# Kernel tuning notes

Measured on AMD Instinct MI355X. Metric: run time of the kernel, lower is better.

The kernel has to match this reference:

```python
import jax, jax.numpy as jnp
import numpy as np

N, T, D_FEAT, D_GATE, D_MODEL = 1024, 32, 158, 63, 256
T_NHEAD, S_NHEAD, BETA = 4, 2, 5.0


def _pe(seq_len, d_model):
    pos = np.arange(seq_len, dtype=np.float32)[:, None]
    div = np.exp(np.arange(0, d_model, 2, dtype=np.float32) * (-np.log(10000.0) / d_model))
    pe = np.zeros((seq_len, d_model), np.float32)
    pe[:, 0::2] = np.sin(pos * div)
    pe[:, 1::2] = np.cos(pos * div)
    return jnp.asarray(pe)


def _ln(x, g, b):
    m = jnp.mean(x, -1, keepdims=True)
    v = jnp.var(x, -1, keepdims=True)
    return (x - m) / jnp.sqrt(v + 1e-5) * g + b


def _attn_block(x, n1g, n1b, Wq, Wk, Wv, n2g, n2b, W1, b1, W2, b2, nhead, over_stocks):
    # Faithful to SAttention/TAttention: per-head split of equally-sized dims is
    # equivalent to a single batched multi-head attention. Dropout p=0 (eval).
    n, t, d = x.shape
    dh = d // nhead
    temp = float(np.sqrt(d / nhead))
    xn = _ln(x, n1g, n1b)
    q = (xn @ Wq).reshape(n, t, nhead, dh)
    k = (xn @ Wk).reshape(n, t, nhead, dh)
    v = (xn @ Wv).reshape(n, t, nhead, dh)
    if over_stocks:
        # attention across stocks, per time step: scores [T,H,N,N]
        s = jnp.einsum('qthd,kthd->thqk', q, k) / temp
        a = jax.nn.softmax(s, -1)
        o = jnp.einsum('thqk,kthd->qthd', a, v).reshape(n, t, d)
    else:
        # attention across time, per stock: scores [N,H,T,T]
        s = jnp.einsum('nqhd,nkhd->nhqk', q, k) / temp
        a = jax.nn.softmax(s, -1)
        o = jnp.einsum('nhqk,nkhd->nqhd', a, v).reshape(n, t, d)
    xt = _ln(xn + o, n2g, n2b)
    ffn = jnp.maximum(xt @ W1 + b1, 0.0) @ W2 + b2
    return xt + ffn


def _forward(x, gate_W, gate_b, feat_W, feat_b, ds_mid_W, ds_mid_b, ds_small_W, ds_small_b,
             tn1g, tn1b, tWq, tWk, tWv, tn2g, tn2b, tW1, tb1, tW2, tb2,
             sn1g, sn1b, sWq, sWk, sWv, sn2g, sn2b, sW1, sb1, sW2, sb2,
             temp_W, fus_W, fus_b, fus_g, fus_bb, dec_W, dec_b):
    src = x[:, :, :D_FEAT]                       # [N,T,158]
    gate_in = x[:, -1, D_FEAT:]                  # [N,63] market features at last step
    g = D_FEAT * jax.nn.softmax((gate_in @ gate_W + gate_b) / BETA, -1)
    src = src * g[:, None, :]
    h = src @ feat_W + feat_b + _pe(T, D_MODEL)  # [N,32,256]
    # multi-scale downsampling: AvgPool1d k=2/s=2 and k=4/s=4 along time
    h_mid = h.reshape(N, T // 2, 2, D_MODEL).mean(2) @ ds_mid_W + ds_mid_b
    h_small = h.reshape(N, T // 4, 4, D_MODEL).mean(2) @ ds_small_W + ds_small_b
    pooled = []
    for hs in (h, h_mid, h_small):
        z = _attn_block(hs, tn1g, tn1b, tWq, tWk, tWv, tn2g, tn2b, tW1, tb1, tW2, tb2,
                        T_NHEAD, over_stocks=False)
        z = _attn_block(z, sn1g, sn1b, sWq, sWk, sWv, sn2g, sn2b, sW1, sb1, sW2, sb2,
                        S_NHEAD, over_stocks=True)
        # TemporalAttention pooling: query = last-step projection
        hh = z @ temp_W
        lam = jax.nn.softmax(jnp.einsum('ntd,nd->nt', hh, hh[:, -1, :]), -1)
        pooled.append(jnp.einsum('nt,ntd->nd', lam, z))
    fused = jnp.concatenate(pooled, -1) @ fus_W + fus_b
    fused = jnp.maximum(_ln(fused, fus_g, fus_bb), 0.0)
    return (fused @ dec_W + dec_b).squeeze(-1)    # [N]


def setup_inputs() -> dict:
    key = jax.random.key(0)
    ks = iter(jax.random.split(key, 40))
    w = lambda shape: jax.random.normal(next(ks), shape, jnp.float32) * 0.02
    d = D_MODEL
    inp = {
        'x': jax.random.normal(next(ks), (N, T, D_FEAT + D_GATE), jnp.float32),
        'gate_W': w((D_GATE, D_FEAT)), 'gate_b': jnp.zeros((D_FEAT,), jnp.float32),
        'feat_W': w((D_FEAT, d)), 'feat_b': jnp.zeros((d,), jnp.float32),
        'ds_mid_W': w((d, d)), 'ds_mid_b': jnp.zeros((d,), jnp.float32),
        'ds_small_W': w((d, d)), 'ds_small_b': jnp.zeros((d,), jnp.float32),
        'tn1g': jnp.ones((d,), jnp.float32), 'tn1b': jnp.zeros((d,), jnp.float32),
        'tWq': w((d, d)), 'tWk': w((d, d)), 'tWv': w((d, d)),
        'tn2g': jnp.ones((d,), jnp.float32), 'tn2b': jnp.zeros((d,), jnp.float32),
        'tW1': w((d, d)), 'tb1': jnp.zeros((d,), jnp.float32),
        'tW2': w((d, d)), 'tb2': jnp.zeros((d,), jnp.float32),
        'sn1g': jnp.ones((d,), jnp.float32), 'sn1b': jnp.zeros((d,), jnp.float32),
        'sWq': w((d, d)), 'sWk': w((d, d)), 'sWv': w((d, d)),
        'sn2g': jnp.ones((d,), jnp.float32), 'sn2b': jnp.zeros((d,), jnp.float32),
        'sW1': w((d, d)), 'sb1': jnp.zeros((d,), jnp.float32),
        'sW2': w((d, d)), 'sb2': jnp.zeros((d,), jnp.float32),
        'temp_W': w((d, d)),
        'fus_W': w((3 * d, d)), 'fus_b': jnp.zeros((d,), jnp.float32),
        'fus_g': jnp.ones((d,), jnp.float32), 'fus_bb': jnp.zeros((d,), jnp.float32),
        'dec_W': w((d, 1)), 'dec_b': jnp.zeros((1,), jnp.float32),
    }
    return inp


def reference(x, gate_W, gate_b, feat_W, feat_b, ds_mid_W, ds_mid_b, ds_small_W, ds_small_b,
              tn1g, tn1b, tWq, tWk, tWv, tn2g, tn2b, tW1, tb1, tW2, tb2,
              sn1g, sn1b, sWq, sWk, sWv, sn2g, sn2b, sW1, sb1, sW2, sb2,
              temp_W, fus_W, fus_b, fus_g, fus_bb, dec_W, dec_b):
    return _forward(x, gate_W, gate_b, feat_W, feat_b, ds_mid_W, ds_mid_b, ds_small_W, ds_small_b,
                    tn1g, tn1b, tWq, tWk, tWv, tn2g, tn2b, tW1, tb1, tW2, tb2,
                    sn1g, sn1b, sWq, sWk, sWv, sn2g, sn2b, sW1, sb1, sW2, sb2,
                    temp_W, fus_W, fus_b, fus_g, fus_bb, dec_W, dec_b)
```

## Files before the change

### kernel.cpp

```cpp
#include <hip/hip_runtime.h>
#include <math.h>

#define NS 1024
#define T0 32
#define DF 158
#define DG 63
#define DM 256
#define XROW (DF + DG)
#define MTOT 57344
#define B1R 32768
#define B2R 49152

typedef unsigned short u16;
typedef __attribute__((ext_vector_type(8))) short bf16x8_t;
typedef __attribute__((ext_vector_type(4))) float f32x4_t;

union frag_u {
  bf16x8_t f;
  unsigned short us[8];
  unsigned int u32[4];
};

__device__ inline unsigned short f2bf(float x) {
  unsigned int u = __float_as_uint(x);
  unsigned int r = u + 0x7fffu + ((u >> 16) & 1u);
  return (unsigned short)(r >> 16);
}
__device__ inline unsigned int pkbf(float lo, float hi) {
  return (unsigned int)f2bf(lo) | ((unsigned int)f2bf(hi) << 16);
}
__device__ inline float bf2f(u16 u) {
  return __uint_as_float(((unsigned int)u) << 16);
}
__device__ inline unsigned int cvtpk(float a, float b) {
  unsigned int r;
  asm("v_cvt_pk_bf16_f32 %0, %1, %2" : "=v"(r) : "v"(a), "v"(b));
  return r;
}

__global__ void k_pe(float* __restrict__ pe) {
  int t = blockIdx.x, d = threadIdx.x;
  int i2 = d & ~1;
  float div = expf((float)i2 * (-logf(10000.0f) / (float)DM));
  float ang = (float)t * div;
  pe[t * DM + d] = (d & 1) ? cosf(ang) : sinf(ang);
}

__global__ void k_gate(const float* __restrict__ x, const float* __restrict__ gW,
                       const float* __restrict__ gb, float* __restrict__ g) {
  int n = blockIdx.x, tid = threadIdx.x;
  __shared__ float gin[DG];
  __shared__ float red[256];
  if (tid < DG) gin[tid] = x[(size_t)n * T0 * XROW + 31 * XROW + DF + tid];
  __syncthreads();
  float myv = 0.f;
  if (tid < DF) {
    float acc = gb[tid];
    for (int j = 0; j < DG; j++) acc = fmaf(gin[j], gW[j * DF + tid], acc);
    myv = acc * (1.0f / 5.0f);
  }
  red[tid] = (tid < DF) ? myv : -1e30f;
  __syncthreads();
  for (int s = 128; s > 0; s >>= 1) { if (tid < s) red[tid] = fmaxf(red[tid], red[tid + s]); __syncthreads(); }
  float mx = red[0];
  __syncthreads();
  float e = (tid < DF) ? expf(myv - mx) : 0.f;
  red[tid] = e;
  __syncthreads();
  for (int s = 128; s > 0; s >>= 1) { if (tid < s) red[tid] += red[tid + s]; __syncthreads(); }
  float sum = red[0];
  if (tid < DF) g[(size_t)n * DF + tid] = (float)DF * e / sum;
}

struct WPrep { const float* s[14]; };
__global__ __launch_bounds__(256) void k_wprep(WPrep w, u16* __restrict__ dst) {
  int mat = blockIdx.x >> 4, nb = blockIdx.x & 15;
  int tid = threadIdx.x;
  int n = nb * 16 + (tid >> 4);
  int kc = (tid & 15) * 16;
  const float* src = w.s[mat];
  int K = (mat == 0) ? DF : 256;
  frag_u f0, f1;
#pragma unroll
  for (int j = 0; j < 8; j++) {
    int k0 = kc + j, k1 = kc + 8 + j;
    f0.us[j] = (k0 < K) ? f2bf(src[(size_t)k0 * 256 + n]) : (u16)0;
    f1.us[j] = (k1 < K) ? f2bf(src[(size_t)k1 * 256 + n]) : (u16)0;
  }
  u16* d = dst + (size_t)mat * 65536 + (size_t)n * 256 + kc;
  *(bf16x8_t*)d = f0.f;
  *(bf16x8_t*)(d + 8) = f1.f;
}

__global__ __launch_bounds__(256) void k_wtrans(const float* __restrict__ W, u16* __restrict__ Wt) {
  __shared__ u16 Ts[64][65];
  int k0 = blockIdx.x * 64, n0 = blockIdx.y * 64;
  int tid = threadIdx.x;
#pragma unroll
  for (int i = 0; i < 16; i++) {
    int e = tid + i * 256;
    int r = e >> 6, c = e & 63;
    Ts[r][c] = f2bf(W[(size_t)(k0 + r) * 256 + n0 + c]);
  }
  __syncthreads();
#pragma unroll
  for (int i = 0; i < 16; i++) {
    int e = tid + i * 256;
    int r = e >> 6, c = e & 63;
    Wt[(size_t)(n0 + r) * 768 + k0 + c] = Ts[c][r];
  }
}

template <bool BIAS, bool RELU, bool RES, bool OUTBF>
__global__ __launch_bounds__(256) void k_bgemm(
    const u16* __restrict__ A,
    const u16* __restrict__ B0, const u16* __restrict__ B1, const u16* __restrict__ B2,
    const float* __restrict__ bias, const u16* __restrict__ res,
    void* __restrict__ C0, void* __restrict__ C1, void* __restrict__ C2) {
  __shared__ __align__(16) unsigned char sm[32768];
  unsigned char* As = sm;
  unsigned char* Bs = sm + 16384;
  const u16* Bt = blockIdx.z == 0 ? B0 : (blockIdx.z == 1 ? B1 : B2);
  void* Cv = blockIdx.z == 0 ? C0 : (blockIdx.z == 1 ? C1 : C2);
  int m0 = blockIdx.y * 128, n0w = blockIdx.x * 128;
  int tid = threadIdx.x, lane = tid & 63, wid = tid >> 6;
  int qi = lane & 15, g = lane >> 4;
  int wr = wid >> 1, wc = wid & 1;
  f32x4_t acc[4][4];
#pragma unroll
  for (int i = 0; i < 4; i++)
#pragma unroll
    for (int j = 0; j < 4; j++) acc[i][j] = (f32x4_t){0.f, 0.f, 0.f, 0.f};
  for (int kt = 0; kt < 4; kt++) {
    if (kt) __syncthreads();
#pragma unroll
    for (int i = 0; i < 4; i++) {
      int cid = tid + i * 256;
      int row = cid >> 3, c = cid & 7;
      int swz = (c * 16) ^ ((row & 7) << 4);
      bf16x8_t va = *(const bf16x8_t*)(A + (size_t)(m0 + row) * 256 + kt * 64 + c * 8);
      *(bf16x8_t*)(As + row * 128 + swz) = va;
      bf16x8_t vb = *(const bf16x8_t*)(Bt + (size_t)(n0w + row) * 256 + kt * 64 + c * 8);
      *(bf16x8_t*)(Bs + row * 128 + swz) = vb;
    }
    __syncthreads();
    bf16x8_t Af[2][4], Bf[2][4];
#pragma unroll
    for (int mi = 0; mi < 4; mi++) {
      int row = wr * 64 + mi * 16 + qi;
      int swz = (row & 7) << 4;
      const unsigned char* ap = As + row * 128;
      Af[0][mi] = *(const bf16x8_t*)(ap + ((g * 16) ^ swz));
      Af[1][mi] = *(const bf16x8_t*)(ap + ((64 + g * 16) ^ swz));
    }
#pragma unroll
    for (int ni = 0; ni < 4; ni++) {
      int row = wc * 64 + ni * 16 + qi;
      int swz = (row & 7) << 4;
      const unsigned char* bp = Bs + row * 128;
      Bf[0][ni] = *(const bf16x8_t*)(bp + ((g * 16) ^ swz));
      Bf[1][ni] = *(const bf16x8_t*)(bp + ((64 + g * 16) ^ swz));
    }
#pragma unroll
    for (int ks = 0; ks < 2; ks++)
#pragma unroll
      for (int mi = 0; mi < 4; mi++)
#pragma unroll
        for (int ni = 0; ni < 4; ni++)
          acc[mi][ni] = __builtin_amdgcn_mfma_f32_16x16x32_bf16(Af[ks][mi], Bf[ks][ni], acc[mi][ni], 0, 0, 0);
  }
#pragma unroll
  for (int mi = 0; mi < 4; mi++) {
#pragma unroll
    for (int ni = 0; ni < 4; ni++) {
#pragma unroll
      for (int r = 0; r < 4; r++) {
        int row = m0 + wr * 64 + mi * 16 + 4 * g + r;
        int col = n0w + wc * 64 + ni * 16 + qi;
        float vv = acc[mi][ni][r];
        if (BIAS) vv += bias[col];
        if (RES) vv += bf2f(res[(size_t)row * 256 + col]);
        if (RELU) vv = fmaxf(vv, 0.f);
        if (OUTBF) ((u16*)Cv)[(size_t)row * 256 + col] = f2bf(vv);
        else ((float*)Cv)[(size_t)row * 256 + col] = vv;
      }
    }
  }
}

__global__ __launch_bounds__(256) void k_fgemm(
    const float* __restrict__ x, const float* __restrict__ gate,
    const u16* __restrict__ Bt, const float* __restrict__ bias,
    const float* __restrict__ pe, float* __restrict__ C) {
  __shared__ __align__(16) unsigned char sm[32768];
  unsigned char* As = sm;
  unsigned char* Bs = sm + 16384;
  int m0 = blockIdx.y * 128, n0w = blockIdx.x * 128;
  int tid = threadIdx.x, lane = tid & 63, wid = tid >> 6;
  int qi = lane & 15, g = lane >> 4;
  int wr = wid >> 1, wc = wid & 1;
  f32x4_t acc[4][4];
#pragma unroll
  for (int i = 0; i < 4; i++)
#pragma unroll
    for (int j = 0; j < 4; j++) acc[i][j] = (f32x4_t){0.f, 0.f, 0.f, 0.f};
  for (int kt = 0; kt < 3; kt++) {
    if (kt) __syncthreads();
#pragma unroll
    for (int i = 0; i < 4; i++) {
      int cid = tid + i * 256;
      int row = cid >> 3, c = cid & 7;
      int swz = (c * 16) ^ ((row & 7) << 4);
      int gk0 = kt * 64 + c * 8;
      const float* xr = x + (size_t)(m0 + row) * XROW;
      const float* gr = gate + (size_t)((m0 + row) >> 5) * DF;
      frag_u f;
#pragma unroll
      for (int j = 0; j < 8; j++) {
        int gk = gk0 + j;
        f.us[j] = (gk < DF) ? f2bf(xr[gk] * gr[gk]) : (u16)0;
      }
      *(bf16x8_t*)(As + row * 128 + swz) = f.f;
      bf16x8_t vb = *(const bf16x8_t*)(Bt + (size_t)(n0w + row) * 256 + kt * 64 + c * 8);
      *(bf16x8_t*)(Bs + row * 128 + swz) = vb;
    }
    __syncthreads();
    bf16x8_t Af[2][4], Bf[2][4];
#pragma unroll
    for (int mi = 0; mi < 4; mi++) {
      int row = wr * 64 + mi * 16 + qi;
      int swz = (row & 7) << 4;
      const unsigned char* ap = As + row * 128;
      Af[0][mi] = *(const bf16x8_t*)(ap + ((g * 16) ^ swz));
      Af[1][mi] = *(const bf16x8_t*)(ap + ((64 + g * 16) ^ swz));
    }
#pragma unroll
    for (int ni = 0; ni < 4; ni++) {
      int row = wc * 64 + ni * 16 + qi;
      int swz = (row & 7) << 4;
      const unsigned char* bp = Bs + row * 128;
      Bf[0][ni] = *(const bf16x8_t*)(bp + ((g * 16) ^ swz));
      Bf[1][ni] = *(const bf16x8_t*)(bp + ((64 + g * 16) ^ swz));
    }
#pragma unroll
    for (int ks = 0; ks < 2; ks++)
#pragma unroll
      for (int mi = 0; mi < 4; mi++)
#pragma unroll
        for (int ni = 0; ni < 4; ni++)
          acc[mi][ni] = __builtin_amdgcn_mfma_f32_16x16x32_bf16(Af[ks][mi], Bf[ks][ni], acc[mi][ni], 0, 0, 0);
  }
#pragma unroll
  for (int mi = 0; mi < 4; mi++) {
#pragma unroll
    for (int ni = 0; ni < 4; ni++) {
#pragma unroll
      for (int r = 0; r < 4; r++) {
        int row = m0 + wr * 64 + mi * 16 + 4 * g + r;
        int col = n0w + wc * 64 + ni * 16 + qi;
        C[(size_t)row * 256 + col] = acc[mi][ni][r] + bias[col] + pe[(row & (T0 - 1)) * DM + col];
      }
    }
  }
}

__global__ __launch_bounds__(256) void k_fus(const u16* __restrict__ A, const u16* __restrict__ Bt,
                                             const float* __restrict__ bias, float* __restrict__ C) {
  __shared__ __align__(16) unsigned char sm[16384];
  unsigned char* As = sm;
  unsigned char* Bs = sm + 8192;
  int n0 = blockIdx.x * 64, m0 = blockIdx.y * 64;
  int tid = threadIdx.x, lane = tid & 63, wid = tid >> 6;
  int qi = lane & 15, g = lane >> 4;
  f32x4_t acc[4];
#pragma unroll
  for (int i = 0; i < 4; i++) acc[i] = (f32x4_t){0.f, 0.f, 0.f, 0.f};
  for (int kt = 0; kt < 12; kt++) {
    if (kt) __syncthreads();
#pragma unroll
    for (int i = 0; i < 2; i++) {
      int cid = tid + i * 256;
      int row = cid >> 3, c = cid & 7;
      int swz = (c * 16) ^ ((row & 7) << 4);
      *(bf16x8_t*)(As + row * 128 + swz) = *(const bf16x8_t*)(A + (size_t)(m0 + row) * 768 + kt * 64 + c * 8);
      *(bf16x8_t*)(Bs + row * 128 + swz) = *(const bf16x8_t*)(Bt + (size_t)(n0 + row) * 768 + kt * 64 + c * 8);
    }
    __syncthreads();
    int arow = wid * 16 + qi;
    int asw = (arow & 7) << 4;
    bf16x8_t Af0 = *(const bf16x8_t*)(As + arow * 128 + ((g * 16) ^ asw));
    bf16x8_t Af1 = *(const bf16x8_t*)(As + arow * 128 + ((64 + g * 16) ^ asw));
#pragma unroll
    for (int ni = 0; ni < 4; ni++) {
      int brow = ni * 16 + qi;
      int bsw = (brow & 7) << 4;
      bf16x8_t B0 = *(const bf16x8_t*)(Bs + brow * 128 + ((g * 16) ^ bsw));
      bf16x8_t B1 = *(const bf16x8_t*)(Bs + brow * 128 + ((64 + g * 16) ^ bsw));
      acc[ni] = __builtin_amdgcn_mfma_f32_16x16x32_bf16(Af0, B0, acc[ni], 0, 0, 0);
      acc[ni] = __builtin_amdgcn_mfma_f32_16x16x32_bf16(Af1, B1, acc[ni], 0, 0, 0);
    }
  }
#pragma unroll
  for (int ni = 0; ni < 4; ni++)
#pragma unroll
    for (int r = 0; r < 4; r++) {
      int row = m0 + wid * 16 + 4 * g + r;
      int col = n0 + ni * 16 + qi;
      C[(size_t)row * 256 + col] = acc[ni][r] + bias[col];
    }
}

template <bool RES, bool ABF>
__global__ __launch_bounds__(256) void k_ln(const void* __restrict__ a, const float* __restrict__ b,
                                            const float* __restrict__ g, const float* __restrict__ be,
                                            u16* __restrict__ out) {
  int row = blockIdx.x * 4 + (threadIdx.x >> 6);
  int lane = threadIdx.x & 63;
  size_t base = (size_t)row * DM + lane * 4;
  float v[4];
  if (ABF) {
    ushort4 u = *(const ushort4*)((const u16*)a + base);
    v[0] = bf2f(u.x); v[1] = bf2f(u.y); v[2] = bf2f(u.z); v[3] = bf2f(u.w);
  } else {
    f32x4_t t = *(const f32x4_t*)((const float*)a + base);
    v[0] = t[0]; v[1] = t[1]; v[2] = t[2]; v[3] = t[3];
  }
  if (RES) {
    f32x4_t t = *(const f32x4_t*)(b + base);
    v[0] += t[0]; v[1] += t[1]; v[2] += t[2]; v[3] += t[3];
  }
  float s = v[0] + v[1] + v[2] + v[3];
#pragma unroll
  for (int off = 1; off < 64; off <<= 1) s += __shfl_xor(s, off);
  float mean = s * (1.0f / DM);
  float d0 = v[0] - mean, d1 = v[1] - mean, d2 = v[2] - mean, d3 = v[3] - mean;
  float ss = d0 * d0 + d1 * d1 + d2 * d2 + d3 * d3;
#pragma unroll
  for (int off = 1; off < 64; off <<= 1) ss += __shfl_xor(ss, off);
  float inv = rsqrtf(ss * (1.0f / DM) + 1e-5f);
  f32x4_t gg = *(const f32x4_t*)(g + lane * 4);
  f32x4_t bb = *(const f32x4_t*)(be + lane * 4);
  ushort4 o4;
  o4.x = f2bf(d0 * inv * gg[0] + bb[0]);
  o4.y = f2bf(d1 * inv * gg[1] + bb[1]);
  o4.z = f2bf(d2 * inv * gg[2] + bb[2]);
  o4.w = f2bf(d3 * inv * gg[3] + bb[3]);
  *(ushort4*)(out + base) = o4;
}

__global__ void k_poolmean(const float* __restrict__ h, u16* __restrict__ out, int Tout, int P) {
  int vi = blockIdx.x * 256 + threadIdx.x;
  int dv = vi & 63;
  int rowi = vi >> 6;
  int to = rowi % Tout;
  int n = rowi / Tout;
  int Tin = Tout * P;
  float s0 = 0.f, s1 = 0.f, s2 = 0.f, s3 = 0.f;
  for (int p = 0; p < P; p++) {
    f32x4_t t = *(const f32x4_t*)(h + ((size_t)(n * Tin + to * P + p)) * DM + dv * 4);
    s0 += t[0]; s1 += t[1]; s2 += t[2]; s3 += t[3];
  }
  float inv = 1.0f / (float)P;
  ushort4 o4;
  o4.x = f2bf(s0 * inv); o4.y = f2bf(s1 * inv); o4.z = f2bf(s2 * inv); o4.w = f2bf(s3 * inv);
  *(ushort4*)(out + (size_t)rowi * DM + dv * 4) = o4;
}

template <int T>
__global__ __launch_bounds__(256) void k_tattn(const u16* __restrict__ q, const u16* __restrict__ k,
                                               const u16* __restrict__ v, float* __restrict__ o) {
  constexpr int TR = (T < 16) ? 16 : T;
  constexpr int QKB = TR * 128;
  constexpr int HS = 2 * QKB + 64 * 80;
  __shared__ __align__(16) unsigned char smem[4 * HS];
  int n = blockIdx.x;
  int tid = threadIdx.x, lane = tid & 63, h = tid >> 6;
  int qi = lane & 15, g = lane >> 4;
  unsigned char* Qs = smem + h * HS;
  unsigned char* Ks = Qs + QKB;
  unsigned char* Vt = Ks + QKB;

  const u16* qh = q + (size_t)n * T * 256 + h * 64;
  const u16* kh = k + (size_t)n * T * 256 + h * 64;
  const u16* vh = v + (size_t)n * T * 256 + h * 64;
  const bf16x8_t zero8 = {0, 0, 0, 0, 0, 0, 0, 0};

  for (int idx = lane; idx < TR * 8; idx += 64) {
    int row = idx >> 3, c = idx & 7;
    bf16x8_t vq = zero8, vk = zero8;
    if (row < T) {
      vq = *(const bf16x8_t*)(qh + (size_t)row * 256 + c * 8);
      vk = *(const bf16x8_t*)(kh + (size_t)row * 256 + c * 8);
    }
    int off = row * 128 + ((c * 16) ^ ((row & 7) << 4));
    *(bf16x8_t*)(Qs + off) = vq;
    *(bf16x8_t*)(Ks + off) = vk;
  }
  {
    int kp = lane & 15, dg = lane >> 4;
    int d0 = dg * 16;
    int kk = 2 * kp;
    int cb = ((((kk >> 2) & 3) << 3) | (((kk >> 4) & 1) << 2) | (kk & 3)) * 2;
    frag_u a0, a1, b0, b1;
    a0.f = a1.f = b0.f = b1.f = zero8;
    if (kk < T) {
      a0.f = *(const bf16x8_t*)(vh + (size_t)kk * 256 + d0);
      a1.f = *(const bf16x8_t*)(vh + (size_t)kk * 256 + d0 + 8);
    }
    if (kk + 1 < T) {
      b0.f = *(const bf16x8_t*)(vh + (size_t)(kk + 1) * 256 + d0);
      b1.f = *(const bf16x8_t*)(vh + (size_t)(kk + 1) * 256 + d0 + 8);
    }
#pragma unroll
    for (int i = 0; i < 8; i++)
      *(unsigned int*)(Vt + (d0 + i) * 80 + cb) = (unsigned int)a0.us[i] | ((unsigned int)b0.us[i] << 16);
#pragma unroll
    for (int i = 0; i < 8; i++)
      *(unsigned int*)(Vt + (d0 + 8 + i) * 80 + cb) = (unsigned int)a1.us[i] | ((unsigned int)b1.us[i] << 16);
  }
  __syncthreads();

  constexpr int NQT = (T == 32) ? 2 : 1;
  constexpr int NSUB = (T == 32) ? 2 : 1;
  const float scale = 0.125f;

  bf16x8_t Qb[NQT][2];
#pragma unroll
  for (int qt = 0; qt < NQT; qt++) {
    int row = qt * 16 + qi;
    int sw = (row & 7) << 4;
#pragma unroll
    for (int kst = 0; kst < 2; kst++)
      Qb[qt][kst] = *(const bf16x8_t*)(Qs + row * 128 + ((kst * 64 + g * 16) ^ sw));
  }
  f32x4_t sacc[NQT][NSUB];
#pragma unroll
  for (int qt = 0; qt < NQT; qt++)
#pragma unroll
    for (int sub = 0; sub < NSUB; sub++) sacc[qt][sub] = (f32x4_t){0.f, 0.f, 0.f, 0.f};
#pragma unroll
  for (int sub = 0; sub < NSUB; sub++) {
    int row = sub * 16 + qi;
    int sw = (row & 7) << 4;
    bf16x8_t Ka[2];
#pragma unroll
    for (int kst = 0; kst < 2; kst++)
      Ka[kst] = *(const bf16x8_t*)(Ks + row * 128 + ((kst * 64 + g * 16) ^ sw));
#pragma unroll
    for (int qt = 0; qt < NQT; qt++)
#pragma unroll
      for (int kst = 0; kst < 2; kst++)
        sacc[qt][sub] = __builtin_amdgcn_mfma_f32_16x16x32_bf16(Ka[kst], Qb[qt][kst], sacc[qt][sub], 0, 0, 0);
  }
  frag_u Pf[NQT];
#pragma unroll
  for (int qt = 0; qt < NQT; qt++) {
    float sv[NSUB][4];
    float mx = -3.0e38f;
#pragma unroll
    for (int sub = 0; sub < NSUB; sub++)
#pragma unroll
      for (int r = 0; r < 4; r++) {
        int key = sub * 16 + 4 * g + r;
        float s = sacc[qt][sub][r] * scale;
        if (key >= T) s = -3.0e38f;
        sv[sub][r] = s;
        mx = fmaxf(mx, s);
      }
    mx = fmaxf(mx, __shfl_xor(mx, 16));
    mx = fmaxf(mx, __shfl_xor(mx, 32));
    float p[NSUB][4];
    float l = 0.f;
#pragma unroll
    for (int sub = 0; sub < NSUB; sub++)
#pragma unroll
      for (int r = 0; r < 4; r++) {
        float e = __expf(sv[sub][r] - mx);
        p[sub][r] = e;
        l += e;
      }
    l += __shfl_xor(l, 16);
    l += __shfl_xor(l, 32);
    float linv = 1.0f / l;
    Pf[qt].u32[0] = cvtpk(p[0][0] * linv, p[0][1] * linv);
    Pf[qt].u32[1] = cvtpk(p[0][2] * linv, p[0][3] * linv);
    if (NSUB == 2) {
      Pf[qt].u32[2] = cvtpk(p[NSUB - 1][0] * linv, p[NSUB - 1][1] * linv);
      Pf[qt].u32[3] = cvtpk(p[NSUB - 1][2] * linv, p[NSUB - 1][3] * linv);
    } else {
      Pf[qt].u32[2] = 0u;
      Pf[qt].u32[3] = 0u;
    }
  }
  f32x4_t oacc[NQT][4];
#pragma unroll
  for (int qt = 0; qt < NQT; qt++)
#pragma unroll
    for (int ni = 0; ni < 4; ni++) oacc[qt][ni] = (f32x4_t){0.f, 0.f, 0.f, 0.f};
#pragma unroll
  for (int ni = 0; ni < 4; ni++) {
    bf16x8_t Vb = *(const bf16x8_t*)(Vt + (ni * 16 + qi) * 80 + g * 16);
#pragma unroll
    for (int qt = 0; qt < NQT; qt++)
      oacc[qt][ni] = __builtin_amdgcn_mfma_f32_16x16x32_bf16(Pf[qt].f, Vb, oacc[qt][ni], 0, 0, 0);
  }
#pragma unroll
  for (int qt = 0; qt < NQT; qt++)
#pragma unroll
    for (int ni = 0; ni < 4; ni++)
#pragma unroll
      for (int r = 0; r < 4; r++) {
        int qq = qt * 16 + 4 * g + r;
        if (qq < T) o[((size_t)(n * T + qq)) * 256 + h * 64 + ni * 16 + qi] = oacc[qt][ni][r];
      }
}

__global__ __launch_bounds__(256) void k_sattn(const u16* __restrict__ q, const u16* __restrict__ k,
                                               const u16* __restrict__ v, float* __restrict__ o) {
  __shared__ __align__(16) unsigned char smem[32768];
  unsigned char* Ks = smem;
  unsigned char* Vt = smem + 16384;

  int bid = blockIdx.x;
  int T, rowbase;
  if (bid < 1024) { T = 32; rowbase = 0; }
  else if (bid < 1536) { T = 16; rowbase = B1R; bid -= 1024; }
  else { T = 8; rowbase = B2R; bid -= 1536; }
  const int NTH = T * 2;
  int xcd = bid & 7, slot = bid >> 3;
  int th = xcd * (NTH >> 3) + (slot >> 4);
  int qb = slot & 15;
  int t = th >> 1, h = th & 1;

  int tid = threadIdx.x;
  int lane = tid & 63;
  int wid = tid >> 6;
  int qi = lane & 15;
  int g = lane >> 4;
  const float invtemp = 0.08838834764831845f;

  const size_t rs = (size_t)T * 256;
  const size_t hb = (size_t)rowbase * 256 + (size_t)t * 256 + h * 128;
  const u16* qp = q + hb;
  const u16* kp = k + hb;
  const u16* vp = v + hb;
  float* op = o + hb;

  int q0 = qb * 64 + wid * 16;

  bf16x8_t Qf[4];
  {
    const u16* src = qp + (size_t)(q0 + qi) * rs + g * 8;
#pragma unroll
    for (int kst = 0; kst < 4; kst++) Qf[kst] = *(const bf16x8_t*)(src + kst * 32);
  }

  f32x4_t Oacc[8];
#pragma unroll
  for (int i = 0; i < 8; i++) Oacc[i] = (f32x4_t){0.f, 0.f, 0.f, 0.f};
  float mrun = -3.0e38f, lrun = 0.f;

  int kpair = tid & 31, dg = tid >> 5;
  int d0s = dg * 16;
  int kk = 2 * kpair;
  int cb = (((kk >> 5) << 5) | (((kk >> 2) & 3) << 3) | (((kk >> 4) & 1) << 2) | (kk & 3)) * 2;

  for (int kb = 0; kb < NS; kb += 64) {
    __syncthreads();
#pragma unroll
    for (int i = 0; i < 4; i++) {
      int cid = tid + i * 256;
      int row = cid >> 4, ch = cid & 15;
      bf16x8_t kv = *(const bf16x8_t*)(kp + (size_t)(kb + row) * rs + ch * 8);
      *(bf16x8_t*)(Ks + row * 256 + ((ch * 16) ^ ((row & 7) << 4))) = kv;
    }
    {
      const u16* s0 = vp + (size_t)(kb + kk) * rs + d0s;
      const u16* s1 = s0 + rs;
      frag_u a0, a1, b0, b1;
      a0.f = *(const bf16x8_t*)s0;
      a1.f = *(const bf16x8_t*)(s0 + 8);
      b0.f = *(const bf16x8_t*)s1;
      b1.f = *(const bf16x8_t*)(s1 + 8);
#pragma unroll
      for (int i = 0; i < 8; i++) {
        int d = d0s + i;
        *(unsigned int*)(Vt + d * 128 + (cb ^ ((d & 7) << 4))) =
            (unsigned int)a0.us[i] | ((unsigned int)b0.us[i] << 16);
      }
#pragma unroll
      for (int i = 0; i < 8; i++) {
        int d = d0s + 8 + i;
        *(unsigned int*)(Vt + d * 128 + (cb ^ ((d & 7) << 4))) =
            (unsigned int)a1.us[i] | ((unsigned int)b1.us[i] << 16);
      }
    }
    __syncthreads();

    f32x4_t sacc[4];
#pragma unroll
    for (int i = 0; i < 4; i++) sacc[i] = (f32x4_t){0.f, 0.f, 0.f, 0.f};
#pragma unroll
    for (int sub = 0; sub < 4; sub++) {
      int row = sub * 16 + qi;
      int swz = (row & 7) << 4;
      const unsigned char* kr = Ks + row * 256;
#pragma unroll
      for (int kst = 0; kst < 4; kst++) {
        bf16x8_t Af = *(const bf16x8_t*)(kr + ((g * 16 + kst * 64) ^ swz));
        sacc[sub] = __builtin_amdgcn_mfma_f32_16x16x32_bf16(Af, Qf[kst], sacc[sub], 0, 0, 0);
      }
    }

    float sv[4][4];
    float pmax = -3.0e38f;
#pragma unroll
    for (int sub = 0; sub < 4; sub++)
#pragma unroll
      for (int r = 0; r < 4; r++) {
        sv[sub][r] = sacc[sub][r] * invtemp;
        pmax = fmaxf(pmax, sv[sub][r]);
      }
    pmax = fmaxf(pmax, __shfl_xor(pmax, 16));
    pmax = fmaxf(pmax, __shfl_xor(pmax, 32));
    if (__any(pmax - mrun > 8.0f)) {
      float mnew = fmaxf(mrun, pmax);
      float fac = __expf(mrun - mnew);
      lrun *= fac;
      float fr[4];
#pragma unroll
      for (int r = 0; r < 4; r++) fr[r] = __shfl(fac, (g << 2) | r);
#pragma unroll
      for (int dsub = 0; dsub < 8; dsub++)
#pragma unroll
        for (int r = 0; r < 4; r++) Oacc[dsub][r] *= fr[r];
      mrun = mnew;
    }
    float p[4][4];
    float ls = 0.f;
#pragma unroll
    for (int sub = 0; sub < 4; sub++)
#pragma unroll
      for (int r = 0; r < 4; r++) {
        float e = __expf(sv[sub][r] - mrun);
        p[sub][r] = e;
        ls += e;
      }
    ls += __shfl_xor(ls, 16);
    ls += __shfl_xor(ls, 32);
    lrun += ls;

    frag_u pf0, pf1;
    pf0.u32[0] = cvtpk(p[0][0], p[0][1]);
    pf0.u32[1] = cvtpk(p[0][2], p[0][3]);
    pf0.u32[2] = cvtpk(p[1][0], p[1][1]);
    pf0.u32[3] = cvtpk(p[1][2], p[1][3]);
    pf1.u32[0] = cvtpk(p[2][0], p[2][1]);
    pf1.u32[1] = cvtpk(p[2][2], p[2][3]);
    pf1.u32[2] = cvtpk(p[3][0], p[3][1]);
    pf1.u32[3] = cvtpk(p[3][2], p[3][3]);

#pragma unroll
    for (int kst = 0; kst < 2; kst++) {
      bf16x8_t Pa = kst ? pf1.f : pf0.f;
#pragma unroll
      for (int dsub = 0; dsub < 8; dsub++) {
        int row = dsub * 16 + qi;
        bf16x8_t Vb = *(const bf16x8_t*)(Vt + row * 128 + ((g * 16 + kst * 64) ^ ((row & 7) << 4)));
        Oacc[dsub] = __builtin_amdgcn_mfma_f32_16x16x32_bf16(Pa, Vb, Oacc[dsub], 0, 0, 0);
      }
    }
  }

  float rin[4];
#pragma unroll
  for (int r = 0; r < 4; r++) rin[r] = 1.0f / __shfl(lrun, (g << 2) | r);
#pragma unroll
  for (int dsub = 0; dsub < 8; dsub++)
#pragma unroll
    for (int r = 0; r < 4; r++) {
      size_t row = (size_t)(q0 + 4 * g + r);
      op[row * rs + dsub * 16 + qi] = Oacc[dsub][r] * rin[r];
    }
}

__global__ __launch_bounds__(256) void k_tpool(const float* __restrict__ hh, const u16* __restrict__ z,
                                               u16* __restrict__ pooled, int T, int off) {
  int n = blockIdx.x, d = threadIdx.x;
  __shared__ float red[256];
  __shared__ float lam[T0];
  __shared__ float lame[T0];
  float last = hh[((size_t)(n * T + T - 1)) * DM + d];
  for (int t = 0; t < T; t++) {
    red[d] = hh[((size_t)(n * T + t)) * DM + d] * last;
    __syncthreads();
    for (int s = 128; s > 0; s >>= 1) { if (d < s) red[d] += red[d + s]; __syncthreads(); }
    if (d == 0) lam[t] = red[0];
    __syncthreads();
  }
  float mx = -1e30f;
  for (int t = 0; t < T; t++) mx = fmaxf(mx, lam[t]);
  if (d < T) lame[d] = expf(lam[d] - mx);
  __syncthreads();
  float sum = 0.f;
  for (int t = 0; t < T; t++) sum += lame[t];
  float acc = 0.f;
  for (int t = 0; t < T; t++) acc += lame[t] * bf2f(z[((size_t)(n * T + t)) * DM + d]);
  pooled[(size_t)n * 768 + off + d] = f2bf(acc / sum);
}

__global__ __launch_bounds__(256) void k_final(const float* __restrict__ f, const float* __restrict__ g,
                                               const float* __restrict__ b, const float* __restrict__ dw,
                                               const float* __restrict__ db, float* __restrict__ out) {
  int n = blockIdx.x, d = threadIdx.x;
  float v = f[(size_t)n * DM + d];
  __shared__ float red[256];
  red[d] = v;
  __syncthreads();
  for (int s = 128; s > 0; s >>= 1) { if (d < s) red[d] += red[d + s]; __syncthreads(); }
  float mean = red[0] * (1.0f / DM);
  __syncthreads();
  float dv = v - mean;
  red[d] = dv * dv;
  __syncthreads();
  for (int s = 128; s > 0; s >>= 1) { if (d < s) red[d] += red[d + s]; __syncthreads(); }
  float var = red[0] * (1.0f / DM);
  __syncthreads();
  float y = dv * rsqrtf(var + 1e-5f) * g[d] + b[d];
  y = fmaxf(y, 0.f);
  red[d] = y * dw[d];
  __syncthreads();
  for (int s = 128; s > 0; s >>= 1) { if (d < s) red[d] += red[d + s]; __syncthreads(); }
  if (d == 0) out[n] = red[0] + db[0];
}

extern "C" void kernel_launch(void* const* d_in, const int* in_sizes, int n_in,
                              void* d_out, int out_size, void* d_ws, size_t ws_size,
                              hipStream_t stream) {
  const float* x = (const float*)d_in[0];
  const float* gate_W = (const float*)d_in[1];
  const float* gate_b = (const float*)d_in[2];
  const float* feat_W = (const float*)d_in[3];
  const float* feat_b = (const float*)d_in[4];
  const float* ds_mid_W = (const float*)d_in[5];
  const float* ds_mid_b = (const float*)d_in[6];
  const float* ds_small_W = (const float*)d_in[7];
  const float* ds_small_b = (const float*)d_in[8];
  const float* tn1g = (const float*)d_in[9];
  const float* tn1b = (const float*)d_in[10];
  const float* tWq = (const float*)d_in[11];
  const float* tWk = (const float*)d_in[12];
  const float* tWv = (const float*)d_in[13];
  const float* tn2g = (const float*)d_in[14];
  const float* tn2b = (const float*)d_in[15];
  const float* tW1 = (const float*)d_in[16];
  const float* tb1 = (const float*)d_in[17];
  const float* tW2 = (const float*)d_in[18];
  const float* tb2 = (const float*)d_in[19];
  const float* sn1g = (const float*)d_in[20];
  const float* sn1b = (const float*)d_in[21];
  const float* sWq = (const float*)d_in[22];
  const float* sWk = (const float*)d_in[23];
  const float* sWv = (const float*)d_in[24];
  const float* sn2g = (const float*)d_in[25];
  const float* sn2b = (const float*)d_in[26];
  const float* sW1 = (const float*)d_in[27];
  const float* sb1 = (const float*)d_in[28];
  const float* sW2 = (const float*)d_in[29];
  const float* sb2 = (const float*)d_in[30];
  const float* temp_W = (const float*)d_in[31];
  const float* fus_W = (const float*)d_in[32];
  const float* fus_b = (const float*)d_in[33];
  const float* fus_g = (const float*)d_in[34];
  const float* fus_bb = (const float*)d_in[35];
  const float* dec_W = (const float*)d_in[36];
  const float* dec_b = (const float*)d_in[37];

  float* ws = (float*)d_ws;
  size_t o = 0;
  float* pe = ws + o; o += 8192;
  float* g = ws + o; o += 161792;
  u16* wt = (u16*)(ws + o); o += 458752;
  float* hcat = ws + o; o += (size_t)MTOT * 256;
  u16* bXNu = (u16*)(ws + o); o += (size_t)MTOT * 128;
  u16* bQu = (u16*)(ws + o); o += (size_t)MTOT * 128;
  u16* bKu = (u16*)(ws + o); o += (size_t)MTOT * 128;
  u16* bVu = (u16*)(ws + o); o += (size_t)MTOT * 128;
  float* bO = hcat;
  float* hh = hcat;
  float* fused = hcat;
  u16* pooledu = bXNu;
  u16* wFus = bKu;

  u16* wFeat = wt;
  u16* wDSm = wt + 1 * 65536;
  u16* wDSs = wt + 2 * 65536;
  u16* wTQ = wt + 3 * 65536;
  u16* wTK = wt + 4 * 65536;
  u16* wTV = wt + 5 * 65536;
  u16* wT1 = wt + 6 * 65536;
  u16* wT2 = wt + 7 * 65536;
  u16* wSQ = wt + 8 * 65536;
  u16* wSK = wt + 9 * 65536;
  u16* wSV = wt + 10 * 65536;
  u16* wS1 = wt + 11 * 65536;
  u16* wS2 = wt + 12 * 65536;
  u16* wTW = wt + 13 * 65536;

  k_pe<<<T0, DM, 0, stream>>>(pe);
  k_gate<<<NS, 256, 0, stream>>>(x, gate_W, gate_b, g);
  WPrep wp;
  wp.s[0] = feat_W; wp.s[1] = ds_mid_W; wp.s[2] = ds_small_W;
  wp.s[3] = tWq; wp.s[4] = tWk; wp.s[5] = tWv; wp.s[6] = tW1; wp.s[7] = tW2;
  wp.s[8] = sWq; wp.s[9] = sWk; wp.s[10] = sWv; wp.s[11] = sW1; wp.s[12] = sW2;
  wp.s[13] = temp_W;
  k_wprep<<<224, 256, 0, stream>>>(wp, wt);

  k_fgemm<<<dim3(2, 256), 256, 0, stream>>>(x, g, wFeat, feat_b, pe, hcat);
  k_poolmean<<<4096, 256, 0, stream>>>(hcat, bQu, 16, 2);
  k_bgemm<true, false, false, false><<<dim3(2, 128, 1), 256, 0, stream>>>(
      bQu, wDSm, wDSm, wDSm, ds_mid_b, nullptr, hcat + (size_t)B1R * 256, nullptr, nullptr);
  k_poolmean<<<2048, 256, 0, stream>>>(hcat, bQu, 8, 4);
  k_bgemm<true, false, false, false><<<dim3(2, 64, 1), 256, 0, stream>>>(
      bQu, wDSs, wDSs, wDSs, ds_small_b, nullptr, hcat + (size_t)B2R * 256, nullptr, nullptr);

  dim3 g1(2, MTOT / 128, 1), g3(2, MTOT / 128, 3);
  k_ln<false, false><<<MTOT / 4, 256, 0, stream>>>(hcat, nullptr, tn1g, tn1b, bXNu);
  k_bgemm<false, false, false, true><<<g3, 256, 0, stream>>>(
      bXNu, wTQ, wTK, wTV, nullptr, nullptr, bQu, bKu, bVu);
  k_tattn<32><<<NS, 256, 0, stream>>>(bQu, bKu, bVu, bO);
  k_tattn<16><<<NS, 256, 0, stream>>>(bQu + (size_t)B1R * 256, bKu + (size_t)B1R * 256,
                                      bVu + (size_t)B1R * 256, bO + (size_t)B1R * 256);
  k_tattn<8><<<NS, 256, 0, stream>>>(bQu + (size_t)B2R * 256, bKu + (size_t)B2R * 256,
                                     bVu + (size_t)B2R * 256, bO + (size_t)B2R * 256);
  k_ln<true, true><<<MTOT / 4, 256, 0, stream>>>(bXNu, bO, tn2g, tn2b, bQu);
  k_bgemm<true, true, false, true><<<g1, 256, 0, stream>>>(
      bQu, wT1, wT1, wT1, tb1, nullptr, bKu, nullptr, nullptr);
  k_bgemm<true, false, true, true><<<g1, 256, 0, stream>>>(
      bKu, wT2, wT2, wT2, tb2, bQu, bVu, nullptr, nullptr);
  k_ln<false, true><<<MTOT / 4, 256, 0, stream>>>(bVu, nullptr, sn1g, sn1b, bXNu);
  k_bgemm<false, false, false, true><<<g3, 256, 0, stream>>>(
      bXNu, wSQ, wSK, wSV, nullptr, nullptr, bQu, bKu, bVu);
  k_sattn<<<1792, 256, 0, stream>>>(bQu, bKu, bVu, bO);
  k_ln<true, true><<<MTOT / 4, 256, 0, stream>>>(bXNu, bO, sn2g, sn2b, bQu);
  k_bgemm<true, true, false, true><<<g1, 256, 0, stream>>>(
      bQu, wS1, wS1, wS1, sb1, nullptr, bKu, nullptr, nullptr);
  k_bgemm<true, false, true, true><<<g1, 256, 0, stream>>>(
      bKu, wS2, wS2, wS2, sb2, bQu, bVu, nullptr, nullptr);
  k_bgemm<false, false, false, false><<<g1, 256, 0, stream>>>(
      bVu, wTW, wTW, wTW, nullptr, nullptr, hh, nullptr, nullptr);
  k_tpool<<<NS, 256, 0, stream>>>(hh, bVu, pooledu, 32, 0);
  k_tpool<<<NS, 256, 0, stream>>>(hh + (size_t)B1R * 256, bVu + (size_t)B1R * 256, pooledu, 16, 256);
  k_tpool<<<NS, 256, 0, stream>>>(hh + (size_t)B2R * 256, bVu + (size_t)B2R * 256, pooledu, 8, 512);

  k_wtrans<<<dim3(12, 4), 256, 0, stream>>>(fus_W, wFus);
  k_fus<<<dim3(4, 16), 256, 0, stream>>>(pooledu, wFus, fus_b, fused);
  k_final<<<NS, 256, 0, stream>>>(fused, fus_g, fus_bb, dec_W, dec_b, (float*)d_out);
}
```

Before: 594.7 us.

## Fold softmax scale into Q weights, double sattn query tiles, async GEMM loads, warp-reduce tpool

Several independent changes land together. The attention temperature and log2(e) are folded into the bf16 Wq weights during prep, so both attention kernels can use exp2 without a per-score multiply. k_sattn now has each wave process two 16-row query tiles that share every K and V fragment read from LDS, which halves the grid and the K/V staging per query. The bgemm tile loads use global_load_lds with the XOR swizzle moved onto the source address. k_tpool replaces its serial block-wide reductions with wave shuffle reductions. Risks include higher register pressure in sattn, lower occupancy, and small rounding differences from pre-scaled bf16 weights.

```diff
diff --git a/kernel.cpp b/kernel.cpp
--- a/kernel.cpp
+++ b/kernel.cpp
@@ -26,9 +26,6 @@
   unsigned int r = u + 0x7fffu + ((u >> 16) & 1u);
   return (unsigned short)(r >> 16);
 }
-__device__ inline unsigned int pkbf(float lo, float hi) {
-  return (unsigned int)f2bf(lo) | ((unsigned int)f2bf(hi) << 16);
-}
 __device__ inline float bf2f(u16 u) {
   return __uint_as_float(((unsigned int)u) << 16);
 }
@@ -36,6 +33,10 @@
   unsigned int r;
   asm("v_cvt_pk_bf16_f32 %0, %1, %2" : "=v"(r) : "v"(a), "v"(b));
   return r;
+}
+__device__ inline void gl16(const u16* gp, unsigned char* lp) {
+  __builtin_amdgcn_global_load_lds((const __attribute__((address_space(1))) unsigned int*)gp,
+                                   (__attribute__((address_space(3))) unsigned int*)lp, 16, 0, 0);
 }
 
 __global__ void k_pe(float* __restrict__ pe) {
@@ -72,20 +73,21 @@
   if (tid < DF) g[(size_t)n * DF + tid] = (float)DF * e / sum;
 }
 
-struct WPrep { const float* s[14]; };
+struct WPrep { const float* s[14]; float sc[14]; };
 __global__ __launch_bounds__(256) void k_wprep(WPrep w, u16* __restrict__ dst) {
   int mat = blockIdx.x >> 4, nb = blockIdx.x & 15;
   int tid = threadIdx.x;
   int n = nb * 16 + (tid >> 4);
   int kc = (tid & 15) * 16;
   const float* src = w.s[mat];
+  float sc = w.sc[mat];
   int K = (mat == 0) ? DF : 256;
   frag_u f0, f1;
 #pragma unroll
   for (int j = 0; j < 8; j++) {
     int k0 = kc + j, k1 = kc + 8 + j;
-    f0.us[j] = (k0 < K) ? f2bf(src[(size_t)k0 * 256 + n]) : (u16)0;
-    f1.us[j] = (k1 < K) ? f2bf(src[(size_t)k1 * 256 + n]) : (u16)0;
+    f0.us[j] = (k0 < K) ? f2bf(src[(size_t)k0 * 256 + n] * sc) : (u16)0;
+    f1.us[j] = (k1 < K) ? f2bf(src[(size_t)k1 * 256 + n] * sc) : (u16)0;
   }
   u16* d = dst + (size_t)mat * 65536 + (size_t)n * 256 + kc;
   *(bf16x8_t*)d = f0.f;
@@ -137,11 +139,9 @@
     for (int i = 0; i < 4; i++) {
       int cid = tid + i * 256;
       int row = cid >> 3, c = cid & 7;
-      int swz = (c * 16) ^ ((row & 7) << 4);
-      bf16x8_t va = *(const bf16x8_t*)(A + (size_t)(m0 + row) * 256 + kt * 64 + c * 8);
-      *(bf16x8_t*)(As + row * 128 + swz) = va;
-      bf16x8_t vb = *(const bf16x8_t*)(Bt + (size_t)(n0w + row) * 256 + kt * 64 + c * 8);
-      *(bf16x8_t*)(Bs + row * 128 + swz) = vb;
+      int cs = c ^ (row & 7);
+      gl16(A + (size_t)(m0 + row) * 256 + kt * 64 + cs * 8, As + cid * 16);
+      gl16(Bt + (size_t)(n0w + row) * 256 + kt * 64 + cs * 8, Bs + cid * 16);
     }
     __syncthreads();
     bf16x8_t Af[2][4], Bf[2][4];
@@ -422,7 +422,6 @@
 
   constexpr int NQT = (T == 32) ? 2 : 1;
   constexpr int NSUB = (T == 32) ? 2 : 1;
-  const float scale = 0.125f;
 
   bf16x8_t Qb[NQT][2];
 #pragma unroll
@@ -462,7 +461,7 @@
 #pragma unroll
       for (int r = 0; r < 4; r++) {
         int key = sub * 16 + 4 * g + r;
-        float s = sacc[qt][sub][r] * scale;
+        float s = sacc[qt][sub][r];
         if (key >= T) s = -3.0e38f;
         sv[sub][r] = s;
         mx = fmaxf(mx, s);
@@ -475,7 +474,7 @@
     for (int sub = 0; sub < NSUB; sub++)
 #pragma unroll
       for (int r = 0; r < 4; r++) {
-        float e = __expf(sv[sub][r] - mx);
+        float e = exp2f(sv[sub][r] - mx);
         p[sub][r] = e;
         l += e;
       }
@@ -523,13 +522,13 @@
 
   int bid = blockIdx.x;
   int T, rowbase;
-  if (bid < 1024) { T = 32; rowbase = 0; }
-  else if (bid < 1536) { T = 16; rowbase = B1R; bid -= 1024; }
-  else { T = 8; rowbase = B2R; bid -= 1536; }
+  if (bid < 512) { T = 32; rowbase = 0; }
+  else if (bid < 768) { T = 16; rowbase = B1R; bid -= 512; }
+  else { T = 8; rowbase = B2R; bid -= 768; }
   const int NTH = T * 2;
   int xcd = bid & 7, slot = bid >> 3;
-  int th = xcd * (NTH >> 3) + (slot >> 4);
-  int qb = slot & 15;
+  int th = xcd * (NTH >> 3) + (slot >> 3);
+  int qb = slot & 7;
   int t = th >> 1, h = th & 1;
 
   int tid = threadIdx.x;
@@ -537,7 +536,6 @@
   int wid = tid >> 6;
   int qi = lane & 15;
   int g = lane >> 4;
-  const float invtemp = 0.08838834764831845f;
 
   const size_t rs = (size_t)T * 256;
   const size_t hb = (size_t)rowbase * 256 + (size_t)t * 256 + h * 128;
@@ -546,19 +544,26 @@
   const u16* vp = v + hb;
   float* op = o + hb;
 
-  int q0 = qb * 64 + wid * 16;
-
-  bf16x8_t Qf[4];
+  int q0 = qb * 128 + wid * 32;
+
+  bf16x8_t QfA[4], QfB[4];
   {
-    const u16* src = qp + (size_t)(q0 + qi) * rs + g * 8;
-#pragma unroll
-    for (int kst = 0; kst < 4; kst++) Qf[kst] = *(const bf16x8_t*)(src + kst * 32);
-  }
-
-  f32x4_t Oacc[8];
-#pragma unroll
-  for (int i = 0; i < 8; i++) Oacc[i] = (f32x4_t){0.f, 0.f, 0.f, 0.f};
-  float mrun = -3.0e38f, lrun = 0.f;
+    const u16* sA = qp + (size_t)(q0 + qi) * rs + g * 8;
+    const u16* sB = sA + 16 * rs;
+#pragma unroll
+    for (int kst = 0; kst < 4; kst++) {
+      QfA[kst] = *(const bf16x8_t*)(sA + kst * 32);
+      QfB[kst] = *(const bf16x8_t*)(sB + kst * 32);
+    }
+  }
+
+  f32x4_t OA[8], OB[8];
+#pragma unroll
+  for (int i = 0; i < 8; i++) {
+    OA[i] = (f32x4_t){0.f, 0.f, 0.f, 0.f};
+    OB[i] = (f32x4_t){0.f, 0.f, 0.f, 0.f};
+  }
+  float mA = -3.0e38f, lA = 0.f, mB = -3.0e38f, lB = 0.f;
 
   int kpair = tid & 31, dg = tid >> 5;
   int d0s = dg * 16;
@@ -597,9 +602,12 @@
     }
     __syncthreads();
 
-    f32x4_t sacc[4];
-#pragma unroll
-    for (int i = 0; i < 4; i++) sacc[i] = (f32x4_t){0.f, 0.f, 0.f, 0.f};
+    f32x4_t saA[4], saB[4];
+#pragma unroll
+    for (int i = 0; i < 4; i++) {
+      saA[i] = (f32x4_t){0.f, 0.f, 0.f, 0.f};
+      saB[i] = (f32x4_t){0.f, 0.f, 0.f, 0.f};
+    }
 #pragma unroll
     for (int sub = 0; sub < 4; sub++) {
       int row = sub * 16 + qi;
@@ -608,105 +616,146 @@
 #pragma unroll
       for (int kst = 0; kst < 4; kst++) {
         bf16x8_t Af = *(const bf16x8_t*)(kr + ((g * 16 + kst * 64) ^ swz));
-        sacc[sub] = __builtin_amdgcn_mfma_f32_16x16x32_bf16(Af, Qf[kst], sacc[sub], 0, 0, 0);
-      }
-    }
-
-    float sv[4][4];
-    float pmax = -3.0e38f;
+        saA[sub] = __builtin_amdgcn_mfma_f32_16x16x32_bf16(Af, QfA[kst], saA[sub], 0, 0, 0);
+        saB[sub] = __builtin_amdgcn_mfma_f32_16x16x32_bf16(Af, QfB[kst], saB[sub], 0, 0, 0);
+      }
+    }
+
+    float pmA = -3.0e38f, pmB = -3.0e38f;
 #pragma unroll
     for (int sub = 0; sub < 4; sub++)
 #pragma unroll
       for (int r = 0; r < 4; r++) {
-        sv[sub][r] = sacc[sub][r] * invtemp;
-        pmax = fmaxf(pmax, sv[sub][r]);
-      }
-    pmax = fmaxf(pmax, __shfl_xor(pmax, 16));
-    pmax = fmaxf(pmax, __shfl_xor(pmax, 32));
-    if (__any(pmax - mrun > 8.0f)) {
-      float mnew = fmaxf(mrun, pmax);
-      float fac = __expf(mrun - mnew);
-      lrun *= fac;
-      float fr[4];
-#pragma unroll
-      for (int r = 0; r < 4; r++) fr[r] = __shfl(fac, (g << 2) | r);
+        pmA = fmaxf(pmA, saA[sub][r]);
+        pmB = fmaxf(pmB, saB[sub][r]);
+      }
+    pmA = fmaxf(pmA, __shfl_xor(pmA, 16));
+    pmA = fmaxf(pmA, __shfl_xor(pmA, 32));
+    pmB = fmaxf(pmB, __shfl_xor(pmB, 16));
+    pmB = fmaxf(pmB, __shfl_xor(pmB, 32));
+    if (__any(fmaxf(pmA - mA, pmB - mB) > 11.5f)) {
+      float mnA = fmaxf(mA, pmA), mnB = fmaxf(mB, pmB);
+      float fA = exp2f(mA - mnA), fB = exp2f(mB - mnB);
+      lA *= fA;
+      lB *= fB;
+      float frA[4], frB[4];
+#pragma unroll
+      for (int r = 0; r < 4; r++) {
+        frA[r] = __shfl(fA, (g << 2) | r);
+        frB[r] = __shfl(fB, (g << 2) | r);
+      }
 #pragma unroll
       for (int dsub = 0; dsub < 8; dsub++)
 #pragma unroll
-        for (int r = 0; r < 4; r++) Oacc[dsub][r] *= fr[r];
-      mrun = mnew;
-    }
-    float p[4][4];
-    float ls = 0.f;
+        for (int r = 0; r < 4; r++) {
+          OA[dsub][r] *= frA[r];
+          OB[dsub][r] *= frB[r];
+        }
+      mA = mnA;
+      mB = mnB;
+    }
+    float pA[4][4], pB[4][4];
+    float lsA = 0.f, lsB = 0.f;
 #pragma unroll
     for (int sub = 0; sub < 4; sub++)
 #pragma unroll
       for (int r = 0; r < 4; r++) {
-        float e = __expf(sv[sub][r] - mrun);
-        p[sub][r] = e;
-        ls += e;
-      }
-    ls += __shfl_xor(ls, 16);
-    ls += __shfl_xor(ls, 32);
-    lrun += ls;
-
-    frag_u pf0, pf1;
-    pf0.u32[0] = cvtpk(p[0][0], p[0][1]);
-    pf0.u32[1] = cvtpk(p[0][2], p[0][3]);
-    pf0.u32[2] = cvtpk(p[1][0], p[1][1]);
-    pf0.u32[3] = cvtpk(p[1][2], p[1][3]);
-    pf1.u32[0] = cvtpk(p[2][0], p[2][1]);
-    pf1.u32[1] = cvtpk(p[2][2], p[2][3]);
-    pf1.u32[2] = cvtpk(p[3][0], p[3][1]);
-    pf1.u32[3] = cvtpk(p[3][2], p[3][3]);
+        float eA = exp2f(saA[sub][r] - mA);
+        float eB = exp2f(saB[sub][r] - mB);
+        pA[sub][r] = eA;
+        pB[sub][r] = eB;
+        lsA += eA;
+        lsB += eB;
+      }
+    lsA += __shfl_xor(lsA, 16);
+    lsA += __shfl_xor(lsA, 32);
+    lsB += __shfl_xor(lsB, 16);
+    lsB += __shfl_xor(lsB, 32);
+    lA += lsA;
+    lB += lsB;
+
+    frag_u fA0, fA1, fB0, fB1;
+    fA0.u32[0] = cvtpk(pA[0][0], pA[0][1]);
+    fA0.u32[1] = cvtpk(pA[0][2], pA[0][3]);
+    fA0.u32[2] = cvtpk(pA[1][0], pA[1][1]);
+    fA0.u32[3] = cvtpk(pA[1][2], pA[1][3]);
+    fA1.u32[0] = cvtpk(pA[2][0], pA[2][1]);
+    fA1.u32[1] = cvtpk(pA[2][2], pA[2][3]);
+    fA1.u32[2] = cvtpk(pA[3][0], pA[3][1]);
+    fA1.u32[3] = cvtpk(pA[3][2], pA[3][3]);
+    fB0.u32[0] = cvtpk(pB[0][0], pB[0][1]);
+    fB0.u32[1] = cvtpk(pB[0][2], pB[0][3]);
+    fB0.u32[2] = cvtpk(pB[1][0], pB[1][1]);
+    fB0.u32[3] = cvtpk(pB[1][2], pB[1][3]);
+    fB1.u32[0] = cvtpk(pB[2][0], pB[2][1]);
+    fB1.u32[1] = cvtpk(pB[2][2], pB[2][3]);
+    fB1.u32[2] = cvtpk(pB[3][0], pB[3][1]);
+    fB1.u32[3] = cvtpk(pB[3][2], pB[3][3]);
 
 #pragma unroll
     for (int kst = 0; kst < 2; kst++) {
-      bf16x8_t Pa = kst ? pf1.f : pf0.f;
+      bf16x8_t PaA = kst ? fA1.f : fA0.f;
+      bf16x8_t PaB = kst ? fB1.f : fB0.f;
 #pragma unroll
       for (int dsub = 0; dsub < 8; dsub++) {
         int row = dsub * 16 + qi;
         bf16x8_t Vb = *(const bf16x8_t*)(Vt + row * 128 + ((g * 16 + kst * 64) ^ ((row & 7) << 4)));
-        Oacc[dsub] = __builtin_amdgcn_mfma_f32_16x16x32_bf16(Pa, Vb, Oacc[dsub], 0, 0, 0);
-      }
-    }
-  }
-
-  float rin[4];
-#pragma unroll
-  for (int r = 0; r < 4; r++) rin[r] = 1.0f / __shfl(lrun, (g << 2) | r);
+        OA[dsub] = __builtin_amdgcn_mfma_f32_16x16x32_bf16(PaA, Vb, OA[dsub], 0, 0, 0);
+        OB[dsub] = __builtin_amdgcn_mfma_f32_16x16x32_bf16(PaB, Vb, OB[dsub], 0, 0, 0);
+      }
+    }
+  }
+
+  float rinA[4], rinB[4];
+#pragma unroll
+  for (int r = 0; r < 4; r++) {
+    rinA[r] = 1.0f / __shfl(lA, (g << 2) | r);
+    rinB[r] = 1.0f / __shfl(lB, (g << 2) | r);
+  }
 #pragma unroll
   for (int dsub = 0; dsub < 8; dsub++)
 #pragma unroll
     for (int r = 0; r < 4; r++) {
-      size_t row = (size_t)(q0 + 4 * g + r);
-      op[row * rs + dsub * 16 + qi] = Oacc[dsub][r] * rin[r];
+      size_t rowA = (size_t)(q0 + 4 * g + r);
+      op[rowA * rs + dsub * 16 + qi] = OA[dsub][r] * rinA[r];
+      op[(rowA + 16) * rs + dsub * 16 + qi] = OB[dsub][r] * rinB[r];
     }
 }
 
 __global__ __launch_bounds__(256) void k_tpool(const float* __restrict__ hh, const u16* __restrict__ z,
                                                u16* __restrict__ pooled, int T, int off) {
-  int n = blockIdx.x, d = threadIdx.x;
-  __shared__ float red[256];
+  int n = blockIdx.x;
+  int tid = threadIdx.x, lane = tid & 63, w = tid >> 6;
   __shared__ float lam[T0];
   __shared__ float lame[T0];
-  float last = hh[((size_t)(n * T + T - 1)) * DM + d];
-  for (int t = 0; t < T; t++) {
-    red[d] = hh[((size_t)(n * T + t)) * DM + d] * last;
-    __syncthreads();
-    for (int s = 128; s > 0; s >>= 1) { if (d < s) red[d] += red[d + s]; __syncthreads(); }
-    if (d == 0) lam[t] = red[0];
-    __syncthreads();
-  }
-  float mx = -1e30f;
-  for (int t = 0; t < T; t++) mx = fmaxf(mx, lam[t]);
-  if (d < T) lame[d] = expf(lam[d] - mx);
-  __syncthreads();
-  float sum = 0.f;
-  for (int t = 0; t < T; t++) sum += lame[t];
+  __shared__ float lsum;
+  const float* hn = hh + (size_t)n * T * DM;
+  f32x4_t last = *(const f32x4_t*)(hn + (size_t)(T - 1) * DM + lane * 4);
+  for (int t = w; t < T; t += 4) {
+    f32x4_t hv = *(const f32x4_t*)(hn + (size_t)t * DM + lane * 4);
+    float s = hv[0] * last[0] + hv[1] * last[1] + hv[2] * last[2] + hv[3] * last[3];
+#pragma unroll
+    for (int o2 = 1; o2 < 64; o2 <<= 1) s += __shfl_xor(s, o2);
+    if (lane == 0) lam[t] = s;
+  }
+  __syncthreads();
+  if (tid < 64) {
+    float vv = (lane < T) ? lam[lane] : -3.0e38f;
+    float mx = vv;
+#pragma unroll
+    for (int o2 = 1; o2 < 64; o2 <<= 1) mx = fmaxf(mx, __shfl_xor(mx, o2));
+    float e = (lane < T) ? expf(vv - mx) : 0.f;
+    float su = e;
+#pragma unroll
+    for (int o2 = 1; o2 < 64; o2 <<= 1) su += __shfl_xor(su, o2);
+    if (lane < T) lame[lane] = e;
+    if (lane == 0) lsum = su;
+  }
+  __syncthreads();
   float acc = 0.f;
-  for (int t = 0; t < T; t++) acc += lame[t] * bf2f(z[((size_t)(n * T + t)) * DM + d]);
-  pooled[(size_t)n * 768 + off + d] = f2bf(acc / sum);
+  const u16* zn = z + (size_t)n * T * DM + tid;
+  for (int t = 0; t < T; t++) acc += lame[t] * bf2f(zn[(size_t)t * DM]);
+  pooled[(size_t)n * 768 + off + tid] = f2bf(acc / lsum);
 }
 
 __global__ __launch_bounds__(256) void k_final(const float* __restrict__ f, const float* __restrict__ g,
@@ -814,6 +863,9 @@
   wp.s[3] = tWq; wp.s[4] = tWk; wp.s[5] = tWv; wp.s[6] = tW1; wp.s[7] = tW2;
   wp.s[8] = sWq; wp.s[9] = sWk; wp.s[10] = sWv; wp.s[11] = sW1; wp.s[12] = sW2;
   wp.s[13] = temp_W;
+  for (int i = 0; i < 14; i++) wp.sc[i] = 1.0f;
+  wp.sc[3] = 0.125f * 1.4426950408889634f;
+  wp.sc[8] = 0.08838834764831845f * 1.4426950408889634f;
   k_wprep<<<224, 256, 0, stream>>>(wp, wt);
 
   k_fgemm<<<dim3(2, 256), 256, 0, stream>>>(x, g, wFeat, feat_b, pe, hcat);
@@ -841,7 +893,7 @@
   k_ln<false, true><<<MTOT / 4, 256, 0, stream>>>(bVu, nullptr, sn1g, sn1b, bXNu);
   k_bgemm<false, false, false, true><<<g3, 256, 0, stream>>>(
       bXNu, wSQ, wSK, wSV, nullptr, nullptr, bQu, bKu, bVu);
-  k_sattn<<<1792, 256, 0, stream>>>(bQu, bKu, bVu, bO);
+  k_sattn<<<896, 256, 0, stream>>>(bQu, bKu, bVu, bO);
   k_ln<true, true><<<MTOT / 4, 256, 0, stream>>>(bXNu, bO, sn2g, sn2b, bQu);
   k_bgemm<true, true, false, true><<<g1, 256, 0, stream>>>(
       bQu, wS1, wS1, wS1, sb1, nullptr, bKu, nullptr, nullptr);
```

After: 497.7 us. -16.3%, faster.
